# Performance work log

Hardware: AMD Instinct MI355X
Metric: run time of the kernel (lower is better)

The kernel has to match this reference:

```python
import jax, jax.numpy as jnp
import numpy as np

# Sizes: N nodes, E directed edges, C input channels, H hidden channels.
N = 50000
E = 800000
C = 64
H = 64
EPS = 1e-5


def _bn(h, gamma, beta):
    # LazyBatchNorm: per-channel normalization over all rows (batch stats).
    m = h.mean(axis=0)
    v = ((h - m) ** 2).mean(axis=0)
    return (h - m) * jax.lax.rsqrt(v + EPS) * gamma + beta


def setup_inputs() -> dict:
    key = jax.random.key(0)
    ks = jax.random.split(key, 8)

    def glorot(k, shape):
        return jax.random.normal(k, shape, dtype=jnp.float32) / jnp.sqrt(jnp.float32(shape[0]))

    x = jax.random.normal(ks[0], (N, C), dtype=jnp.float32)
    edge_index = jax.random.randint(ks[1], (2, E), 0, N)
    return {
        "x": x,
        "edge_index": edge_index,
        "W_unite": glorot(ks[2], (2 * C, H)),
        "b_unite": jnp.zeros((H,), jnp.float32),
        "g1": jnp.ones((H,), jnp.float32),
        "be1": jnp.zeros((H,), jnp.float32),
        "W_gconv": glorot(ks[3], (2 * H, H)),
        "b_gconv": jnp.zeros((H,), jnp.float32),
        "g2": jnp.ones((H,), jnp.float32),
        "be2": jnp.zeros((H,), jnp.float32),
        "W_transfer": glorot(ks[4], (2 * H, H)),
        "b_transfer": jnp.zeros((H,), jnp.float32),
        "W_lin": glorot(ks[5], (H, H)),
        "b_lin": jnp.zeros((H,), jnp.float32),
        "g3": jnp.ones((H,), jnp.float32),
        "be3": jnp.zeros((H,), jnp.float32),
    }


def reference(x, edge_index, W_unite, b_unite, g1, be1, W_gconv, b_gconv, g2, be2,
              W_transfer, b_transfer, W_lin, b_lin, g3, be3):
    n = x.shape[0]
    src_e = edge_index[0]
    dst_e = edge_index[1]
    # linmaps1: ptensors0 -> ptensors1 with singleton reference domains (identity on data).
    # unite1: each node's domain becomes {node} U N(node). Row layout: first n rows
    # are self rows (atom i in domain i), then E rows (atom src in domain dst).
    self_idx = jnp.arange(n)
    rows_src = jnp.concatenate([self_idx, src_e])   # atom index per row
    rows_dom = jnp.concatenate([self_idx, dst_e])   # domain owner per row

    # --- unite1 (2 linmaps: gather + broadcast-of-domain-sum), then linear + BN + relu
    f = x[rows_src]                                           # [R, C] gather
    dsum = jax.ops.segment_sum(f, rows_dom, num_segments=n)   # [N, C]
    h = jnp.concatenate([f, dsum[rows_dom]], axis=-1) @ W_unite + b_unite  # [R, H]
    h = jax.nn.relu(_bn(h, g1, be1))
    # dropout1: identity in eval mode

    # --- higher graph conv: reduce each domain to order-0, aggregate over edges,
    # broadcast back and combine with local rows (2 maps), linear + BN + relu
    s = jax.ops.segment_sum(h, rows_dom, num_segments=n)          # [N, H] per-domain reduce
    msg = jax.ops.segment_sum(s[src_e], dst_e, num_segments=n)    # [N, H] neighborhood sum
    h2 = jnp.concatenate([h, msg[rows_dom]], axis=-1) @ W_gconv + b_gconv  # [R, H]
    h2 = jax.nn.relu(_bn(h2, g2, be2))
    # dropout2: identity

    # --- transfer back to ptensors0 (singleton domains): per-atom reduce over all rows
    # referencing that atom + the atom's own self row (2 maps), linear + BN + relu.
    # NOTE: the source reuses batchnorm2 here (it is assigned twice in __init__).
    agg = jax.ops.segment_sum(h2, rows_src, num_segments=n)       # [N, H]
    t = jnp.concatenate([h2[:n], agg], axis=-1) @ W_transfer + b_transfer  # [N, H]
    t = jax.nn.relu(_bn(t, g2, be2))
    # dropout3: identity

    # --- final linear + relu, BN + relu
    out = jax.nn.relu(t @ W_lin + b_lin)
    out = jax.nn.relu(_bn(out, g3, be3))
    # dropout4: identity
    return out
```

## Files before the change

kernel.cpp:

```cpp
#include <hip/hip_runtime.h>
#include <cstdint>
#include <math.h>

#define NN 50000
#define EE 800000
#define RR 850000
#define NT_N 3125
#define NT_R 53125
#define NBLK_H2 2048
#define NBLK_MM 512
#define CHUNK 512
#define NCH 98

typedef short  bf16x8 __attribute__((ext_vector_type(8)));
typedef float  f32x4  __attribute__((ext_vector_type(4)));

__device__ __forceinline__ float bf2f(unsigned short b) {
    unsigned int u = ((unsigned int)b) << 16;
    return __builtin_bit_cast(float, u);
}
__device__ __forceinline__ unsigned short f2bf(float f) {
    unsigned int u = __builtin_bit_cast(unsigned int, f);
    u = u + 0x7fffu + ((u >> 16) & 1u);
    return (unsigned short)(u >> 16);
}
__device__ __forceinline__ void atomAddD(double* p, double v) { unsafeAtomicAdd(p, v); }
__device__ __forceinline__ int atomAddI(int* p, int v) { return atomicAdd(p, v); }

__device__ __forceinline__ void split8(const float* p, bf16x8& hi, bf16x8& lo) {
    f32x4 v0 = *reinterpret_cast<const f32x4*>(p);
    f32x4 v1 = *reinterpret_cast<const f32x4*>(p + 4);
#pragma unroll
    for (int j = 0; j < 4; j++) {
        unsigned short h0 = f2bf(v0[j]);
        hi[j] = (short)h0; lo[j] = (short)f2bf(v0[j] - bf2f(h0));
        unsigned short h1 = f2bf(v1[j]);
        hi[4 + j] = (short)h1; lo[4 + j] = (short)f2bf(v1[j] - bf2f(h1));
    }
}
__device__ __forceinline__ void split8r(const float* v, bf16x8& hi, bf16x8& lo) {
#pragma unroll
    for (int j = 0; j < 8; j++) {
        unsigned short h = f2bf(v[j]);
        hi[j] = (short)h; lo[j] = (short)f2bf(v[j] - bf2f(h));
    }
}

template <bool RELU, bool STATS>
__device__ __forceinline__ void epi_tile(float* wl, int lane, const f32x4* acc,
                                         const float* bv, float* __restrict__ gout,
                                         int tile, double* ssum, double* ssq) {
    const int m = lane & 15, quad = lane >> 4;
#pragma unroll
    for (int ct = 0; ct < 4; ct++)
#pragma unroll
        for (int i = 0; i < 4; i++) {
            float val = acc[ct][i] + bv[ct];
            if (RELU) val = fmaxf(val, 0.f);
            wl[(quad * 4 + i) * 68 + ct * 16 + m] = val;
            if (STATS) { ssum[ct] += (double)val; ssq[ct] += (double)val * (double)val; }
        }
    asm volatile("s_waitcnt lgkmcnt(0)" ::: "memory");
#pragma unroll
    for (int j = 0; j < 4; j++) {
        int row = j * 4 + quad;
        f32x4 vv = *reinterpret_cast<const f32x4*>(wl + row * 68 + m * 4);
        *reinterpret_cast<f32x4*>(gout + ((size_t)(tile << 4) + row) * 64 + m * 4) = vv;
    }
}

__device__ __forceinline__ void epi_tile_b16(float* wl, int lane, const f32x4* acc,
                                             unsigned short* __restrict__ gout, int tile) {
    const int m = lane & 15, quad = lane >> 4;
#pragma unroll
    for (int ct = 0; ct < 4; ct++)
#pragma unroll
        for (int i = 0; i < 4; i++)
            wl[(quad * 4 + i) * 68 + ct * 16 + m] = acc[ct][i];
    asm volatile("s_waitcnt lgkmcnt(0)" ::: "memory");
#pragma unroll
    for (int j = 0; j < 4; j++) {
        int row = j * 4 + quad;
        f32x4 vv = *reinterpret_cast<const f32x4*>(wl + row * 68 + m * 4);
        unsigned int p0 = (unsigned int)f2bf(vv[0]) | ((unsigned int)f2bf(vv[1]) << 16);
        unsigned int p1 = (unsigned int)f2bf(vv[2]) | ((unsigned int)f2bf(vv[3]) << 16);
        uint2 pk; pk.x = p0; pk.y = p1;
        *reinterpret_cast<uint2*>(gout + ((size_t)(tile << 4) + row) * 64 + m * 4) = pk;
    }
}

__device__ __forceinline__ void stats_block_out(float* ldsbase, int lane, int wid,
                                                const double* ssum, const double* ssq,
                                                double* __restrict__ part) {
    const int m = lane & 15, quad = lane >> 4;
    double* dl = (double*)ldsbase;
    __syncthreads();
#pragma unroll
    for (int ct = 0; ct < 4; ct++) {
        double sv = ssum[ct], qv = ssq[ct];
        sv += __shfl_xor(sv, 16, 64); sv += __shfl_xor(sv, 32, 64);
        qv += __shfl_xor(qv, 16, 64); qv += __shfl_xor(qv, 32, 64);
        if (quad == 0) {
            dl[wid * 128 + ct * 16 + m]      = sv;
            dl[wid * 128 + 64 + ct * 16 + m] = qv;
        }
    }
    __syncthreads();
    int tid = wid * 64 + lane;
    if (tid < 128) {
        double tot = dl[tid] + dl[128 + tid] + dl[256 + tid] + dl[384 + tid];
        part[(size_t)blockIdx.x * 128 + tid] = tot;
    }
}

__global__ void k_red(const double* __restrict__ p, int nblk, double* __restrict__ raw) {
    int t = threadIdx.x;
    double acc = 0.0;
    for (int b = blockIdx.x; b < nblk; b += gridDim.x)
        acc += p[(size_t)b * 128 + t];
    atomAddD(&raw[t], acc);
}

__global__ void k_degx(const int* __restrict__ ei, int* __restrict__ od, int* __restrict__ id,
                       const float* __restrict__ x, unsigned short* __restrict__ xb) {
    int i = blockIdx.x * 256 + threadIdx.x;
    xb[i] = f2bf(x[i]);
    if (i < EE) {
        atomAddI(&od[ei[i]], 1);
        atomAddI(&id[ei[EE + i]], 1);
    }
}

__global__ void k_scanA(const int* __restrict__ id, const int* __restrict__ od,
                        int* __restrict__ csum) {
    int arr = blockIdx.x / NCH;
    int ch  = blockIdx.x % NCH;
    const int* cnt = arr ? od : id;
    int t = threadIdx.x;
    int i0 = ch * CHUNK + t;
    int s = 0;
    if (i0 < NN) s += cnt[i0];
    if (i0 + 256 < NN && (t + 256) < CHUNK) s += cnt[i0 + 256];
#pragma unroll
    for (int d = 1; d < 64; d <<= 1) s += __shfl_xor(s, d, 64);
    __shared__ int ws[4];
    if ((t & 63) == 0) ws[t >> 6] = s;
    __syncthreads();
    if (t == 0) csum[arr * NCH + ch] = ws[0] + ws[1] + ws[2] + ws[3];
}

__global__ void k_scanB(int* __restrict__ csum) {
    __shared__ int part[256];
    int t = threadIdx.x;
    int arr = t >> 7, slot = t & 127;
    int v = (slot < NCH) ? csum[arr * NCH + slot] : 0;
    part[t] = v;
    __syncthreads();
#pragma unroll
    for (int d = 1; d < 128; d <<= 1) {
        int val = (slot >= d) ? part[t - d] : 0;
        __syncthreads();
        part[t] += val;
        __syncthreads();
    }
    if (slot < NCH)
        csum[arr * NCH + slot] = (slot == 0) ? 0 : part[t - 1];
}

__global__ void k_scanC(const int* __restrict__ id, const int* __restrict__ od,
                        const int* __restrict__ csum,
                        int* __restrict__ off, int* __restrict__ cursor,
                        int* __restrict__ off_s, int* __restrict__ cursor_s) {
    int arr = blockIdx.x / NCH;
    int ch  = blockIdx.x % NCH;
    const int* cnt = arr ? od : id;
    int* o  = arr ? off_s : off;
    int* cu = arr ? cursor_s : cursor;
    int t = threadIdx.x;
    int idx = ch * CHUNK + 2 * t;
    int e0 = 0, e1 = 0;
    if (idx < NN)     e0 = cnt[idx];
    if (idx + 1 < NN) e1 = cnt[idx + 1];
    int p = e0 + e1;
    int lane = t & 63;
    int incl = p;
#pragma unroll
    for (int d = 1; d < 64; d <<= 1) {
        int v = __shfl_up(incl, d, 64);
        if (lane >= d) incl += v;
    }
    __shared__ int wsum[4];
    if (lane == 63) wsum[t >> 6] = incl;
    __syncthreads();
    int w = t >> 6;
    int wbase = 0;
#pragma unroll
    for (int i = 0; i < 4; i++) if (i < w) wbase += wsum[i];
    int base = csum[arr * NCH + ch] + wbase + (incl - p);
    if (idx < NN)     { o[idx]     = base;      cu[idx]     = base; }
    if (idx + 1 < NN) { o[idx + 1] = base + e0; cu[idx + 1] = base + e0; }
    if (blockIdx.x == 0 && t == 0) { off[NN] = EE; off_s[NN] = EE; }
}

__global__ void k_fill(const int* __restrict__ ei, int* __restrict__ cursor,
                       unsigned int* __restrict__ sd_s) {
    int e = blockIdx.x * 256 + threadIdx.x;
    int s = ei[e], d = ei[EE + e];
    int p = atomAddI(&cursor[d], 1);
    sd_s[p] = (unsigned int)s | ((unsigned int)d << 16);
}

__global__ void k_fill2(const unsigned int* __restrict__ sd_s, int* __restrict__ cursor_s,
                        int* __restrict__ perm_s) {
    int p = blockIdx.x * 256 + threadIdx.x;
    int s = (int)(sd_s[p] & 0xFFFFu);
    int q = atomAddI(&cursor_s[s], 1);
    perm_s[q] = p;
}

__global__ void k_dsum_csr(const float* __restrict__ x, const unsigned short* __restrict__ xb,
                           const int* __restrict__ off,
                           const unsigned int* __restrict__ sd_s, float* __restrict__ dsum) {
    int team = (blockIdx.x * 256 + threadIdx.x) >> 6;
    int c = threadIdx.x & 63;
    float a[16];
#pragma unroll
    for (int j = 0; j < 16; j++) a[j] = 0.f;
    a[0] = x[(size_t)team * 64 + c];
    int e = off[team], e1 = off[team + 1];
    for (; e + 15 < e1; e += 16)
#pragma unroll
        for (int j = 0; j < 16; j++) a[j] += bf2f(xb[(size_t)(sd_s[e + j] & 0xFFFFu) * 64 + c]);
    for (; e + 3 < e1; e += 4)
#pragma unroll
        for (int j = 0; j < 4; j++) a[j] += bf2f(xb[(size_t)(sd_s[e + j] & 0xFFFFu) * 64 + c]);
    for (; e < e1; e++) a[0] += bf2f(xb[(size_t)(sd_s[e] & 0xFFFFu) * 64 + c]);
#pragma unroll
    for (int j = 0; j < 8; j++) a[j] += a[j + 8];
#pragma unroll
    for (int j = 0; j < 4; j++) a[j] += a[j + 4];
    dsum[(size_t)team * 64 + c] = (a[0] + a[1]) + (a[2] + a[3]);
}

__global__ void k_uv3(const float* __restrict__ x, const float* __restrict__ dsum,
                      const float* __restrict__ W,
                      const int* __restrict__ od, const int* __restrict__ id,
                      unsigned short* __restrict__ ub, float* __restrict__ v,
                      double* __restrict__ part) {
    __shared__ float lds[4][16 * 68];
    const int lane = threadIdx.x & 63;
    const int wid_ = threadIdx.x >> 6;
    const int m = lane & 15, quad = lane >> 4;
    const int gwave = (blockIdx.x * blockDim.x + threadIdx.x) >> 6;
    const int nwaves = (gridDim.x * blockDim.x) >> 6;
    float* wl = lds[wid_];

    bf16x8 wfh[4][4], wfl[4][4];
#pragma unroll
    for (int kk = 0; kk < 4; kk++)
#pragma unroll
        for (int ct = 0; ct < 4; ct++) {
            float wv[8];
#pragma unroll
            for (int j = 0; j < 8; j++)
                wv[j] = W[(kk * 32 + quad * 8 + j) * 64 + ct * 16 + m];
            split8r(wv, wfh[kk][ct], wfl[kk][ct]);
        }
    float zb[4] = {0.f, 0.f, 0.f, 0.f};
    double ssum[4] = {0,0,0,0}, ssq[4] = {0,0,0,0};

    for (int tile = gwave; tile < NT_N; tile += nwaves) {
        const int r = (tile << 4) + m;
        bf16x8 ah[4], al[4];
        split8(x    + (size_t)r * 64 + quad * 8,      ah[0], al[0]);
        split8(x    + (size_t)r * 64 + 32 + quad * 8, ah[1], al[1]);
        split8(dsum + (size_t)r * 64 + quad * 8,      ah[2], al[2]);
        split8(dsum + (size_t)r * 64 + 32 + quad * 8, ah[3], al[3]);

        f32x4 zero = {0.f, 0.f, 0.f, 0.f};
        f32x4 aU[4], aV[4], aU2[4];
#pragma unroll
        for (int ct = 0; ct < 4; ct++) {
            aU[ct] = zero; aV[ct] = zero; aU2[ct] = zero;
#pragma unroll
            for (int kk = 0; kk < 2; kk++) {
                aU[ct]  = __builtin_amdgcn_mfma_f32_16x16x32_bf16(al[kk],   wfh[kk][ct],   aU[ct],  0, 0, 0);
                aU[ct]  = __builtin_amdgcn_mfma_f32_16x16x32_bf16(ah[kk],   wfl[kk][ct],   aU[ct],  0, 0, 0);
                aU[ct]  = __builtin_amdgcn_mfma_f32_16x16x32_bf16(ah[kk],   wfh[kk][ct],   aU[ct],  0, 0, 0);
                aV[ct]  = __builtin_amdgcn_mfma_f32_16x16x32_bf16(al[kk+2], wfh[kk+2][ct], aV[ct],  0, 0, 0);
                aV[ct]  = __builtin_amdgcn_mfma_f32_16x16x32_bf16(ah[kk+2], wfl[kk+2][ct], aV[ct],  0, 0, 0);
                aV[ct]  = __builtin_amdgcn_mfma_f32_16x16x32_bf16(ah[kk+2], wfh[kk+2][ct], aV[ct],  0, 0, 0);
                aU2[ct] = __builtin_amdgcn_mfma_f32_16x16x32_bf16(al[kk+2], wfh[kk][ct],   aU2[ct], 0, 0, 0);
                aU2[ct] = __builtin_amdgcn_mfma_f32_16x16x32_bf16(ah[kk+2], wfl[kk][ct],   aU2[ct], 0, 0, 0);
                aU2[ct] = __builtin_amdgcn_mfma_f32_16x16x32_bf16(ah[kk+2], wfh[kk][ct],   aU2[ct], 0, 0, 0);
            }
        }

#pragma unroll
        for (int i = 0; i < 4; i++) {
            int r2 = (tile << 4) + quad * 4 + i;
            double wod = 1.0 + od[r2], wgt = 1.0 + id[r2];
#pragma unroll
            for (int ct = 0; ct < 4; ct++) {
                double uu = aU[ct][i], vv = aV[ct][i], u2v = aU2[ct][i];
                ssum[ct] += wod * uu + wgt * vv;
                ssq[ct]  += wod * uu * uu + wgt * vv * vv + 2.0 * vv * u2v;
            }
        }

        epi_tile_b16(wl, lane, aU, ub, tile);
        epi_tile<false, false>(wl, lane, aV, zb, v, tile, nullptr, nullptr);
    }

    stats_block_out(&lds[0][0], lane, wid_, ssum, ssq, part);
}

__global__ void k_fin1(const double* __restrict__ raw, const float* __restrict__ b,
                       float* __restrict__ fin, double inv_cnt) {
    int c = threadIdx.x;
    double m1 = raw[c] * inv_cnt;
    double var = raw[64 + c] * inv_cnt - m1 * m1;
    if (var < 0.0) var = 0.0;
    fin[c] = (float)(m1 + (double)b[c]);
    fin[64 + c] = (float)(1.0 / sqrt(var + 1e-5));
}

__global__ void k_fin(const double* __restrict__ raw, float* __restrict__ fin, double inv_cnt) {
    int c = threadIdx.x;
    double mean = raw[c] * inv_cnt;
    double var = raw[64 + c] * inv_cnt - mean * mean;
    if (var < 0.0) var = 0.0;
    fin[c] = (float)mean;
    fin[64 + c] = (float)(1.0 / sqrt(var + 1e-5));
}

__global__ void k_s1h(const unsigned short* __restrict__ ub, const float* __restrict__ v,
                      const int* __restrict__ off, const unsigned int* __restrict__ sd_s,
                      const float* __restrict__ b_un, const float* __restrict__ fin,
                      const float* __restrict__ g1, const float* __restrict__ be1,
                      unsigned short* __restrict__ stb, unsigned short* __restrict__ hb) {
    int team = (blockIdx.x * 256 + threadIdx.x) >> 6;
    int c = threadIdx.x & 63;
    float sc = fin[64 + c] * g1[c];
    float tsh = (b_un[c] - fin[c]) * sc + be1[c];
    float vn = v[(size_t)team * 64 + c];
    float a[16];
#pragma unroll
    for (int j = 0; j < 16; j++) a[j] = 0.f;
    float hs = fmaxf((bf2f(ub[(size_t)team * 64 + c]) + vn) * sc + tsh, 0.f);
    a[0] = hs;
    hb[(size_t)team * 64 + c] = f2bf(hs);
    int e = off[team], e1 = off[team + 1];
    for (; e + 15 < e1; e += 16)
#pragma unroll
        for (int j = 0; j < 16; j++) {
            float h = fmaxf((bf2f(ub[(size_t)(sd_s[e + j] & 0xFFFFu) * 64 + c]) + vn) * sc + tsh, 0.f);
            a[j] += h;
            hb[(size_t)(NN + e + j) * 64 + c] = f2bf(h);
        }
    for (; e + 3 < e1; e += 4)
#pragma unroll
        for (int j = 0; j < 4; j++) {
            float h = fmaxf((bf2f(ub[(size_t)(sd_s[e + j] & 0xFFFFu) * 64 + c]) + vn) * sc + tsh, 0.f);
            a[j] += h;
            hb[(size_t)(NN + e + j) * 64 + c] = f2bf(h);
        }
    for (; e < e1; e++) {
        float h = fmaxf((bf2f(ub[(size_t)(sd_s[e] & 0xFFFFu) * 64 + c]) + vn) * sc + tsh, 0.f);
        a[0] += h;
        hb[(size_t)(NN + e) * 64 + c] = f2bf(h);
    }
#pragma unroll
    for (int j = 0; j < 8; j++) a[j] += a[j + 8];
#pragma unroll
    for (int j = 0; j < 4; j++) a[j] += a[j + 4];
    stb[(size_t)team * 64 + c] = f2bf((a[0] + a[1]) + (a[2] + a[3]));
}

__global__ void k_msg_csr(const int* __restrict__ off, const unsigned int* __restrict__ sd_s,
                          const unsigned short* __restrict__ stb, float* __restrict__ msg) {
    int team = (blockIdx.x * 256 + threadIdx.x) >> 6;
    int c = threadIdx.x & 63;
    float a[16];
#pragma unroll
    for (int j = 0; j < 16; j++) a[j] = 0.f;
    int e = off[team], e1 = off[team + 1];
    for (; e + 15 < e1; e += 16)
#pragma unroll
        for (int j = 0; j < 16; j++) a[j] += bf2f(stb[(size_t)(sd_s[e + j] & 0xFFFFu) * 64 + c]);
    for (; e + 3 < e1; e += 4)
#pragma unroll
        for (int j = 0; j < 4; j++) a[j] += bf2f(stb[(size_t)(sd_s[e + j] & 0xFFFFu) * 64 + c]);
    for (; e < e1; e++) a[0] += bf2f(stb[(size_t)(sd_s[e] & 0xFFFFu) * 64 + c]);
#pragma unroll
    for (int j = 0; j < 8; j++) a[j] += a[j + 8];
#pragma unroll
    for (int j = 0; j < 4; j++) a[j] += a[j + 4];
    msg[(size_t)team * 64 + c] = (a[0] + a[1]) + (a[2] + a[3]);
}

__global__ void k_mb(const float* __restrict__ in, float* __restrict__ outp,
                     const float* __restrict__ W) {
    __shared__ float lds[4][16 * 68];
    const int lane = threadIdx.x & 63;
    const int wid = threadIdx.x >> 6;
    const int m = lane & 15, quad = lane >> 4;
    const int gwave = (blockIdx.x * blockDim.x + threadIdx.x) >> 6;
    const int nwaves = (gridDim.x * blockDim.x) >> 6;
    float* wl = lds[wid];

    bf16x8 wfh[2][4], wfl[2][4];
#pragma unroll
    for (int kk = 0; kk < 2; kk++)
#pragma unroll
        for (int ct = 0; ct < 4; ct++) {
            float wv[8];
#pragma unroll
            for (int j = 0; j < 8; j++)
                wv[j] = W[(kk * 32 + quad * 8 + j) * 64 + ct * 16 + m];
            split8r(wv, wfh[kk][ct], wfl[kk][ct]);
        }
    float zb[4] = {0.f, 0.f, 0.f, 0.f};

    for (int tile = gwave; tile < NT_N; tile += nwaves) {
        const int r = (tile << 4) + m;
        bf16x8 ah[2], al[2];
        split8(in + (size_t)r * 64 + quad * 8,      ah[0], al[0]);
        split8(in + (size_t)r * 64 + 32 + quad * 8, ah[1], al[1]);

        f32x4 zero = {0.f, 0.f, 0.f, 0.f};
        f32x4 acc[4];
#pragma unroll
        for (int ct = 0; ct < 4; ct++) {
            acc[ct] = zero;
#pragma unroll
            for (int kk = 0; kk < 2; kk++) {
                acc[ct] = __builtin_amdgcn_mfma_f32_16x16x32_bf16(al[kk], wfh[kk][ct], acc[ct], 0, 0, 0);
                acc[ct] = __builtin_amdgcn_mfma_f32_16x16x32_bf16(ah[kk], wfl[kk][ct], acc[ct], 0, 0, 0);
                acc[ct] = __builtin_amdgcn_mfma_f32_16x16x32_bf16(ah[kk], wfh[kk][ct], acc[ct], 0, 0, 0);
            }
        }
        epi_tile<false, false>(wl, lane, acc, zb, outp, tile, nullptr, nullptr);
    }
}

__global__ void k_h2(const unsigned short* __restrict__ hb, unsigned short* __restrict__ h2b,
                     const float* __restrict__ mb, const unsigned int* __restrict__ sd_s,
                     const float* __restrict__ W, const float* __restrict__ b_gc,
                     double* __restrict__ part) {
    __shared__ float lds[4][16 * 68];
    const int lane = threadIdx.x & 63;
    const int wid = threadIdx.x >> 6;
    const int m = lane & 15, quad = lane >> 4;
    const int gwave = (blockIdx.x * blockDim.x + threadIdx.x) >> 6;
    const int nwaves = (gridDim.x * blockDim.x) >> 6;
    float* wl = lds[wid];

    bf16x8 wfh[2][4], wfl[2][4];
#pragma unroll
    for (int kk = 0; kk < 2; kk++)
#pragma unroll
        for (int ct = 0; ct < 4; ct++) {
            float wv[8];
#pragma unroll
            for (int j = 0; j < 8; j++)
                wv[j] = W[(kk * 32 + quad * 8 + j) * 64 + ct * 16 + m];
            split8r(wv, wfh[kk][ct], wfl[kk][ct]);
        }

    float bv[4];
#pragma unroll
    for (int ct = 0; ct < 4; ct++) bv[ct] = b_gc[ct * 16 + m];

    double ssum[4] = {0,0,0,0}, ssq[4] = {0,0,0,0};

    for (int tile = gwave; tile < NT_R; tile += nwaves) {
        const int r = (tile << 4) + m;
        int dm = (tile < NT_N) ? r : (int)(sd_s[r - NN] >> 16);

        bf16x8 ah[2];
        ah[0] = *reinterpret_cast<const bf16x8*>(hb + (size_t)r * 64 + quad * 8);
        ah[1] = *reinterpret_cast<const bf16x8*>(hb + (size_t)r * 64 + 32 + quad * 8);

        f32x4 zero = {0.f, 0.f, 0.f, 0.f};
        f32x4 acc[4];
#pragma unroll
        for (int ct = 0; ct < 4; ct++) {
            acc[ct] = zero;
#pragma unroll
            for (int kk = 0; kk < 2; kk++) {
                acc[ct] = __builtin_amdgcn_mfma_f32_16x16x32_bf16(ah[kk], wfl[kk][ct], acc[ct], 0, 0, 0);
                acc[ct] = __builtin_amdgcn_mfma_f32_16x16x32_bf16(ah[kk], wfh[kk][ct], acc[ct], 0, 0, 0);
            }
        }

#pragma unroll
        for (int i = 0; i < 4; i++) {
            int dmv = __shfl(dm, (lane & 48) + quad * 4 + i, 64);
#pragma unroll
            for (int ct = 0; ct < 4; ct++) {
                float val = acc[ct][i] + bv[ct] + mb[(size_t)dmv * 64 + ct * 16 + m];
                wl[(quad * 4 + i) * 68 + ct * 16 + m] = val;
                ssum[ct] += (double)val;
                ssq[ct]  += (double)val * (double)val;
            }
        }
        asm volatile("s_waitcnt lgkmcnt(0)" ::: "memory");
#pragma unroll
        for (int j = 0; j < 4; j++) {
            int row = j * 4 + quad;
            f32x4 vv = *reinterpret_cast<const f32x4*>(wl + row * 68 + m * 4);
            unsigned int p0 = (unsigned int)f2bf(vv[0]) | ((unsigned int)f2bf(vv[1]) << 16);
            unsigned int p1 = (unsigned int)f2bf(vv[2]) | ((unsigned int)f2bf(vv[3]) << 16);
            uint2 pk; pk.x = p0; pk.y = p1;
            *reinterpret_cast<uint2*>(h2b + ((size_t)(tile << 4) + row) * 64 + m * 4) = pk;
        }
    }

    stats_block_out(&lds[0][0], lane, wid, ssum, ssq, part);
}

__global__ void k_agg_csr(const unsigned short* __restrict__ h2b, const int* __restrict__ off_s,
                          const int* __restrict__ perm_s, const float* __restrict__ fin2,
                          const float* __restrict__ g2, const float* __restrict__ be2,
                          unsigned short* __restrict__ aggb) {
    int n = (blockIdx.x * 256 + threadIdx.x) >> 6;
    int c = threadIdx.x & 63;
    float sc = fin2[64 + c] * g2[c];
    float sh = be2[c] - fin2[c] * sc;
    float a[16];
#pragma unroll
    for (int j = 0; j < 16; j++) a[j] = 0.f;
    a[0] = fmaxf(bf2f(h2b[(size_t)n * 64 + c]) * sc + sh, 0.f);
    int q = off_s[n], q1 = off_s[n + 1];
    for (; q + 15 < q1; q += 16)
#pragma unroll
        for (int j = 0; j < 16; j++) {
            float hv = bf2f(h2b[(size_t)(NN + perm_s[q + j]) * 64 + c]);
            a[j] += fmaxf(hv * sc + sh, 0.f);
        }
    for (; q + 3 < q1; q += 4)
#pragma unroll
        for (int j = 0; j < 4; j++) {
            float hv = bf2f(h2b[(size_t)(NN + perm_s[q + j]) * 64 + c]);
            a[j] += fmaxf(hv * sc + sh, 0.f);
        }
    for (; q < q1; q++) {
        float hv = bf2f(h2b[(size_t)(NN + perm_s[q]) * 64 + c]);
        a[0] += fmaxf(hv * sc + sh, 0.f);
    }
#pragma unroll
    for (int j = 0; j < 8; j++) a[j] += a[j + 8];
#pragma unroll
    for (int j = 0; j < 4; j++) a[j] += a[j + 4];
    aggb[(size_t)n * 64 + c] = f2bf((a[0] + a[1]) + (a[2] + a[3]));
}

__global__ void k_mm3(const unsigned short* __restrict__ h2b, const unsigned short* __restrict__ aggb,
                      const float* __restrict__ W, const float* __restrict__ bias,
                      const float* __restrict__ fin2, const float* __restrict__ g2,
                      const float* __restrict__ be2,
                      float* __restrict__ outp, double* __restrict__ part) {
    __shared__ float lds[4][16 * 68];
    const int lane = threadIdx.x & 63;
    const int wid = threadIdx.x >> 6;
    const int m = lane & 15, quad = lane >> 4;
    const int gwave = (blockIdx.x * blockDim.x + threadIdx.x) >> 6;
    const int nwaves = (gridDim.x * blockDim.x) >> 6;
    float* wl = lds[wid];

    bf16x8 wfh[4][4], wfl[4][4];
#pragma unroll
    for (int kk = 0; kk < 4; kk++)
#pragma unroll
        for (int ct = 0; ct < 4; ct++) {
            float wv[8];
#pragma unroll
            for (int j = 0; j < 8; j++)
                wv[j] = W[(kk * 32 + quad * 8 + j) * 64 + ct * 16 + m];
            split8r(wv, wfh[kk][ct], wfl[kk][ct]);
        }

    float bv[4];
#pragma unroll
    for (int ct = 0; ct < 4; ct++) bv[ct] = bias[ct * 16 + m];

    float s2f[2][8], t2f[2][8];
#pragma unroll
    for (int kk = 0; kk < 2; kk++)
#pragma unroll
        for (int j = 0; j < 8; j++) {
            int c = kk * 32 + quad * 8 + j;
            float sc = fin2[64 + c] * g2[c];
            s2f[kk][j] = sc;
            t2f[kk][j] = be2[c] - fin2[c] * sc;
        }

    double ssum[4] = {0,0,0,0}, ssq[4] = {0,0,0,0};

    for (int tile = gwave; tile < NT_N; tile += nwaves) {
        const int r = (tile << 4) + m;
        bf16x8 ah[4], al[2];
#pragma unroll
        for (int kk = 0; kk < 2; kk++) {
            bf16x8 hv = *reinterpret_cast<const bf16x8*>(h2b + (size_t)r * 64 + kk * 32 + quad * 8);
            float tv[8];
#pragma unroll
            for (int j = 0; j < 8; j++) {
                float f = bf2f((unsigned short)hv[j]);
                tv[j] = fmaxf(f * s2f[kk][j] + t2f[kk][j], 0.f);
            }
            split8r(tv, ah[kk], al[kk]);
        }
        ah[2] = *reinterpret_cast<const bf16x8*>(aggb + (size_t)r * 64 + quad * 8);
        ah[3] = *reinterpret_cast<const bf16x8*>(aggb + (size_t)r * 64 + 32 + quad * 8);

        f32x4 zero = {0.f, 0.f, 0.f, 0.f};
        f32x4 acc[4];
#pragma unroll
        for (int ct = 0; ct < 4; ct++) {
            acc[ct] = zero;
#pragma unroll
            for (int kk = 0; kk < 2; kk++)
                acc[ct] = __builtin_amdgcn_mfma_f32_16x16x32_bf16(al[kk], wfh[kk][ct], acc[ct], 0, 0, 0);
#pragma unroll
            for (int kk = 0; kk < 4; kk++)
                acc[ct] = __builtin_amdgcn_mfma_f32_16x16x32_bf16(ah[kk], wfl[kk][ct], acc[ct], 0, 0, 0);
#pragma unroll
            for (int kk = 0; kk < 4; kk++)
                acc[ct] = __builtin_amdgcn_mfma_f32_16x16x32_bf16(ah[kk], wfh[kk][ct], acc[ct], 0, 0, 0);
        }

        epi_tile<false, true>(wl, lane, acc, bv, outp, tile, ssum, ssq);
    }

    stats_block_out(&lds[0][0], lane, wid, ssum, ssq, part);
}

__global__ void k_mm4(const float* __restrict__ tpre, const float* __restrict__ W,
                      const float* __restrict__ bias, const float* __restrict__ fin3,
                      const float* __restrict__ g2, const float* __restrict__ be2,
                      float* __restrict__ outp, double* __restrict__ part) {
    __shared__ float lds[4][16 * 68];
    const int lane = threadIdx.x & 63;
    const int wid = threadIdx.x >> 6;
    const int m = lane & 15, quad = lane >> 4;
    const int gwave = (blockIdx.x * blockDim.x + threadIdx.x) >> 6;
    const int nwaves = (gridDim.x * blockDim.x) >> 6;
    float* wl = lds[wid];

    bf16x8 wfh[2][4], wfl[2][4];
#pragma unroll
    for (int kk = 0; kk < 2; kk++)
#pragma unroll
        for (int ct = 0; ct < 4; ct++) {
            float wv[8];
#pragma unroll
            for (int j = 0; j < 8; j++)
                wv[j] = W[(kk * 32 + quad * 8 + j) * 64 + ct * 16 + m];
            split8r(wv, wfh[kk][ct], wfl[kk][ct]);
        }

    float bv[4];
#pragma unroll
    for (int ct = 0; ct < 4; ct++) bv[ct] = bias[ct * 16 + m];

    float sc[2][8], sh[2][8];
#pragma unroll
    for (int kk = 0; kk < 2; kk++)
#pragma unroll
        for (int j = 0; j < 8; j++) {
            int c = kk * 32 + quad * 8 + j;
            float s = fin3[64 + c] * g2[c];
            sc[kk][j] = s;
            sh[kk][j] = be2[c] - fin3[c] * s;
        }

    double ssum[4] = {0,0,0,0}, ssq[4] = {0,0,0,0};

    for (int tile = gwave; tile < NT_N; tile += nwaves) {
        const int r = (tile << 4) + m;
        bf16x8 ah[2], al[2];
#pragma unroll
        for (int kk = 0; kk < 2; kk++) {
            f32x4 v0 = *reinterpret_cast<const f32x4*>(tpre + (size_t)r * 64 + kk * 32 + quad * 8);
            f32x4 v1 = *reinterpret_cast<const f32x4*>(tpre + (size_t)r * 64 + kk * 32 + quad * 8 + 4);
            float tv[8];
#pragma unroll
            for (int j = 0; j < 4; j++) {
                tv[j]     = fmaxf(v0[j] * sc[kk][j]     + sh[kk][j],     0.f);
                tv[4 + j] = fmaxf(v1[j] * sc[kk][4 + j] + sh[kk][4 + j], 0.f);
            }
            split8r(tv, ah[kk], al[kk]);
        }

        f32x4 zero = {0.f, 0.f, 0.f, 0.f};
        f32x4 acc[4];
#pragma unroll
        for (int ct = 0; ct < 4; ct++) {
            acc[ct] = zero;
#pragma unroll
            for (int kk = 0; kk < 2; kk++) {
                acc[ct] = __builtin_amdgcn_mfma_f32_16x16x32_bf16(al[kk], wfh[kk][ct], acc[ct], 0, 0, 0);
                acc[ct] = __builtin_amdgcn_mfma_f32_16x16x32_bf16(ah[kk], wfl[kk][ct], acc[ct], 0, 0, 0);
                acc[ct] = __builtin_amdgcn_mfma_f32_16x16x32_bf16(ah[kk], wfh[kk][ct], acc[ct], 0, 0, 0);
            }
        }

        epi_tile<true, true>(wl, lane, acc, bv, outp, tile, ssum, ssq);
    }

    stats_block_out(&lds[0][0], lane, wid, ssum, ssq, part);
}

__global__ void k_out(const float* __restrict__ op, const float* __restrict__ fin,
                      const float* __restrict__ g, const float* __restrict__ be,
                      float* __restrict__ out) {
    int i = blockIdx.x * 256 + threadIdx.x;
    int c = i & 63;
    out[i] = fmaxf((op[i] - fin[c]) * fin[64 + c] * g[c] + be[c], 0.f);
}

extern "C" void kernel_launch(void* const* d_in, const int* in_sizes, int n_in,
                              void* d_out, int out_size, void* d_ws, size_t ws_size,
                              hipStream_t stream) {
    const float* x    = (const float*)d_in[0];
    const int*   ei   = (const int*)d_in[1];
    const float* W_un = (const float*)d_in[2];
    const float* b_un = (const float*)d_in[3];
    const float* g1   = (const float*)d_in[4];
    const float* be1  = (const float*)d_in[5];
    const float* W_gc = (const float*)d_in[6];
    const float* b_gc = (const float*)d_in[7];
    const float* g2   = (const float*)d_in[8];
    const float* be2  = (const float*)d_in[9];
    const float* W_tr = (const float*)d_in[10];
    const float* b_tr = (const float*)d_in[11];
    const float* W_li = (const float*)d_in[12];
    const float* b_li = (const float*)d_in[13];
    const float* g3   = (const float*)d_in[14];
    const float* be3  = (const float*)d_in[15];

    float* ws = (float*)d_ws;
    const size_t FN = (size_t)NN * 64;
    const size_t FR = (size_t)RR * 64;
    float* P0 = ws;
    float* P1 = ws + FN;
    float* P2 = ws + 2 * FN;
    float* H  = ws + 3 * FN;
    unsigned short* ub   = (unsigned short*)P0;
    float* v      = P1;
    unsigned short* stb  = (unsigned short*)P2;
    int*   csum   = (int*)P2;
    double* part_uv = (double*)P2;
    float* dsum   = H;
    unsigned short* xb16 = (unsigned short*)(H + FN);
    unsigned short* hb  = (unsigned short*)H;
    unsigned short* h2b = (unsigned short*)H + FR;
    float* msg    = P0;
    unsigned short* aggb = (unsigned short*)P1;
    float* tpre   = P2;
    float* outpre = P0;
    double* part_h2 = (double*)P2;
    double* part_m3 = (double*)P0;
    double* part_m4 = (double*)P1;
    double*       stats_raw = (double*)(H + FR);
    int*          od        = (int*)(stats_raw + 512);
    int*          id        = od + NN;
    int*          off       = id + NN;
    int*          cursor    = off + NN + 1;
    int*          off_s     = cursor + NN;
    int*          cursor_s  = off_s + NN + 1;
    unsigned int* sd_s      = (unsigned int*)(cursor_s + NN);
    int*          perm_s    = (int*)(sd_s + EE);
    float*        stats_fin = (float*)(perm_s + EE);

    hipMemsetAsync(stats_raw, 0, 512 * sizeof(double) + 2 * NN * sizeof(int), stream);

    k_degx <<<12500, 256, 0, stream>>>(ei, od, id, x, xb16);
    k_scanA<<<2 * NCH, 256, 0, stream>>>(id, od, csum);
    k_scanB<<<1, 256, 0, stream>>>(csum);
    k_scanC<<<2 * NCH, 256, 0, stream>>>(id, od, csum, off, cursor, off_s, cursor_s);
    k_fill <<<3125, 256, 0, stream>>>(ei, cursor, sd_s);
    k_fill2<<<3125, 256, 0, stream>>>(sd_s, cursor_s, perm_s);

    k_dsum_csr<<<12500, 256, 0, stream>>>(x, xb16, off, sd_s, dsum);
    k_uv3<<<NBLK_MM, 256, 0, stream>>>(x, dsum, W_un, od, id, ub, v, part_uv);
    k_red<<<16, 128, 0, stream>>>(part_uv, NBLK_MM, stats_raw + 0);
    k_fin1<<<1, 64, 0, stream>>>(stats_raw + 0, b_un, stats_fin + 0, 1.0 / (double)RR);

    k_s1h<<<12500, 256, 0, stream>>>(ub, v, off, sd_s, b_un, stats_fin + 0, g1, be1,
                                     stb, hb);
    k_msg_csr<<<12500, 256, 0, stream>>>(off, sd_s, stb, msg);
    k_mb<<<512, 256, 0, stream>>>(msg, msg, W_gc + 64 * 64);

    k_h2<<<NBLK_H2, 256, 0, stream>>>(hb, h2b, msg, sd_s, W_gc, b_gc, part_h2);
    k_red<<<32, 128, 0, stream>>>(part_h2, NBLK_H2, stats_raw + 128);
    k_fin<<<1, 64, 0, stream>>>(stats_raw + 128, stats_fin + 128, 1.0 / (double)RR);
    k_agg_csr<<<12500, 256, 0, stream>>>(h2b, off_s, perm_s, stats_fin + 128, g2, be2, aggb);

    k_mm3<<<NBLK_MM, 256, 0, stream>>>(h2b, aggb, W_tr, b_tr, stats_fin + 128, g2, be2,
                                       tpre, part_m3);
    k_red<<<16, 128, 0, stream>>>(part_m3, NBLK_MM, stats_raw + 256);
    k_fin<<<1, 64, 0, stream>>>(stats_raw + 256, stats_fin + 256, 1.0 / (double)NN);

    k_mm4<<<NBLK_MM, 256, 0, stream>>>(tpre, W_li, b_li, stats_fin + 256, g2, be2,
                                       outpre, part_m4);
    k_red<<<16, 128, 0, stream>>>(part_m4, NBLK_MM, stats_raw + 384);
    k_fin<<<1, 64, 0, stream>>>(stats_raw + 384, stats_fin + 384, 1.0 / (double)NN);

    k_out<<<12500, 256, 0, stream>>>(outpre, stats_fin + 384, g3, be3, (float*)d_out);
}
```

Measured before the change: 689.0 us.

## Prefetch next tile's inputs and use float per-lane BN stat accumulators in gconv kernel

The gconv MFMA kernel now software-pipelines its tile loop: the next tile's domain index and bf16 activation fragments are loaded before the current tile's MFMA and epilogue run, hiding global load latency. Per-lane batch-norm sum and sum-of-squares accumulation switches from double to float, converted to double only before the block reduction. This cuts FP64 ALU work in the inner loop but raises register pressure and loses some accumulation precision, since each lane sums many rows in float.

```diff
diff --git a/kernel.cpp b/kernel.cpp
--- a/kernel.cpp
+++ b/kernel.cpp
@@ -472,37 +472,49 @@
 #pragma unroll
     for (int ct = 0; ct < 4; ct++) bv[ct] = b_gc[ct * 16 + m];
 
-    double ssum[4] = {0,0,0,0}, ssq[4] = {0,0,0,0};
-
-    for (int tile = gwave; tile < NT_R; tile += nwaves) {
+    float fsum[4] = {0.f,0.f,0.f,0.f}, fsq[4] = {0.f,0.f,0.f,0.f};
+
+    int tile = gwave;
+    bf16x8 c0, c1;
+    int cdm = 0;
+    if (tile < NT_R) {
         const int r = (tile << 4) + m;
-        int dm = (tile < NT_N) ? r : (int)(sd_s[r - NN] >> 16);
-
-        bf16x8 ah[2];
-        ah[0] = *reinterpret_cast<const bf16x8*>(hb + (size_t)r * 64 + quad * 8);
-        ah[1] = *reinterpret_cast<const bf16x8*>(hb + (size_t)r * 64 + 32 + quad * 8);
+        cdm = (tile < NT_N) ? r : (int)(sd_s[r - NN] >> 16);
+        c0 = *reinterpret_cast<const bf16x8*>(hb + (size_t)r * 64 + quad * 8);
+        c1 = *reinterpret_cast<const bf16x8*>(hb + (size_t)r * 64 + 32 + quad * 8);
+    }
+
+    for (; tile < NT_R; tile += nwaves) {
+        const int tn = tile + nwaves;
+        bf16x8 n0 = c0, n1 = c1;
+        int ndm = cdm;
+        if (tn < NT_R) {
+            const int rn = (tn << 4) + m;
+            ndm = (tn < NT_N) ? rn : (int)(sd_s[rn - NN] >> 16);
+            n0 = *reinterpret_cast<const bf16x8*>(hb + (size_t)rn * 64 + quad * 8);
+            n1 = *reinterpret_cast<const bf16x8*>(hb + (size_t)rn * 64 + 32 + quad * 8);
+        }
 
         f32x4 zero = {0.f, 0.f, 0.f, 0.f};
         f32x4 acc[4];
 #pragma unroll
         for (int ct = 0; ct < 4; ct++) {
             acc[ct] = zero;
-#pragma unroll
-            for (int kk = 0; kk < 2; kk++) {
-                acc[ct] = __builtin_amdgcn_mfma_f32_16x16x32_bf16(ah[kk], wfl[kk][ct], acc[ct], 0, 0, 0);
-                acc[ct] = __builtin_amdgcn_mfma_f32_16x16x32_bf16(ah[kk], wfh[kk][ct], acc[ct], 0, 0, 0);
-            }
+            acc[ct] = __builtin_amdgcn_mfma_f32_16x16x32_bf16(c0, wfl[0][ct], acc[ct], 0, 0, 0);
+            acc[ct] = __builtin_amdgcn_mfma_f32_16x16x32_bf16(c0, wfh[0][ct], acc[ct], 0, 0, 0);
+            acc[ct] = __builtin_amdgcn_mfma_f32_16x16x32_bf16(c1, wfl[1][ct], acc[ct], 0, 0, 0);
+            acc[ct] = __builtin_amdgcn_mfma_f32_16x16x32_bf16(c1, wfh[1][ct], acc[ct], 0, 0, 0);
         }
 
 #pragma unroll
         for (int i = 0; i < 4; i++) {
-            int dmv = __shfl(dm, (lane & 48) + quad * 4 + i, 64);
+            int dmv = __shfl(cdm, (lane & 48) + quad * 4 + i, 64);
 #pragma unroll
             for (int ct = 0; ct < 4; ct++) {
                 float val = acc[ct][i] + bv[ct] + mb[(size_t)dmv * 64 + ct * 16 + m];
                 wl[(quad * 4 + i) * 68 + ct * 16 + m] = val;
-                ssum[ct] += (double)val;
-                ssq[ct]  += (double)val * (double)val;
+                fsum[ct] += val;
+                fsq[ct]  += val * val;
             }
         }
         asm volatile("s_waitcnt lgkmcnt(0)" ::: "memory");
@@ -515,9 +527,14 @@
             uint2 pk; pk.x = p0; pk.y = p1;
             *reinterpret_cast<uint2*>(h2b + ((size_t)(tile << 4) + row) * 64 + m * 4) = pk;
         }
-    }
-
-    stats_block_out(&lds[0][0], lane, wid, ssum, ssq, part);
+
+        c0 = n0; c1 = n1; cdm = ndm;
+    }
+
+    double dsum[4], dsq[4];
+#pragma unroll
+    for (int ct = 0; ct < 4; ct++) { dsum[ct] = (double)fsum[ct]; dsq[ct] = (double)fsq[ct]; }
+    stats_block_out(&lds[0][0], lane, wid, dsum, dsq, part);
 }
 
 __global__ void k_agg_csr(const unsigned short* __restrict__ h2b, const int* __restrict__ off_s,
```

Result: faster. 666.8 us, median of 2 (-3.2%).
